# Optimization experiments

Hardware: AMD Instinct MI355X
Metric: run time of the kernel (lower is better)

The kernel has to match this reference:

```python
import jax, jax.numpy as jnp
import numpy as np

N = 50000      # nodes
E = 600000     # edges
F_IN = 128
F_OUT = 128
R = 4          # num_relations
BN_EPS = 1e-5  # PyTorch BatchNorm1d default


def setup_inputs() -> dict:
    key = jax.random.key(0)
    ks = jax.random.split(key, 8)
    s = 1.0 / np.sqrt(F_IN)
    return {
        "x": jax.random.normal(ks[0], (N, F_IN), jnp.float32),
        "edge_index": jax.random.randint(ks[1], (2, E), 0, N),
        "edge_type": jax.random.randint(ks[2], (E,), 0, R),
        "W_self": jax.random.uniform(ks[3], (F_IN, F_OUT), jnp.float32, -s, s),
        "b_self": jnp.zeros((F_OUT,), jnp.float32),
        "W1": jax.random.uniform(ks[4], (R, F_IN, F_OUT), jnp.float32, -s, s),
        "b1": jnp.zeros((R, F_OUT), jnp.float32),
        "gamma": jnp.ones((R, F_OUT), jnp.float32),
        "beta": jnp.zeros((R, F_OUT), jnp.float32),
        "W2": jax.random.uniform(ks[5], (R, F_OUT, F_OUT), jnp.float32, -s, s),
        "b2": jnp.zeros((R, F_OUT), jnp.float32),
    }


def reference(x, edge_index, edge_type, W_self, b_self, W1, b1, gamma, beta, W2, b2):
    row, col = edge_index[0], edge_index[1]
    # Per-relation scatter-add aggregation in one segment_sum pass:
    # segment id = relation * N + destination row.
    seg = edge_type * N + row
    agg = jax.ops.segment_sum(x[col], seg, num_segments=R * N)
    agg = agg.reshape(R, N, F_IN)
    # GIN update with eps=0: h_r = x + agg_r
    h = x[None, :, :] + agg                              # (R, N, F_IN)
    # Per-relation MLP: Linear -> BatchNorm(train stats) -> ReLU -> Linear
    h = jnp.einsum('rnf,rfo->rno', h, W1) + b1[:, None, :]
    mean = jnp.mean(h, axis=1, keepdims=True)
    var = jnp.var(h, axis=1, keepdims=True)              # biased, as in BN
    h = (h - mean) * jax.lax.rsqrt(var + BN_EPS)
    h = h * gamma[:, None, :] + beta[:, None, :]
    h = jax.nn.relu(h)
    h = jnp.einsum('rno,rop->rnp', h, W2) + b2[:, None, :]
    # Self-loop linear plus sum over relations
    return x @ W_self + b_self + jnp.sum(h, axis=0)
```

## Files before the change

kernel.cpp:

```cpp
#include <hip/hip_runtime.h>

#define Nn 50000
#define Ee 600000
#define Rr 4
#define NSEG (Rr * Nn)
#define NBIN 200704
#define BN_EPS 1e-5f
#define ECAP 2048

typedef __bf16 bfrag  __attribute__((ext_vector_type(8)));
typedef float  f32x4  __attribute__((ext_vector_type(4)));

__device__ __forceinline__ unsigned short f2b(float f) {
    union { float f; unsigned int u; } v; v.f = f;
    return (unsigned short)((v.u + 0x7FFFu + ((v.u >> 16) & 1u)) >> 16);
}
__device__ __forceinline__ float b2f(unsigned short u) {
    union { unsigned int u; float f; } v; v.u = ((unsigned int)u) << 16; return v.f;
}

__global__ __launch_bounds__(256) void prep_k(
    const float* __restrict__ x, const float* __restrict__ W1,
    const float* __restrict__ W2, const float* __restrict__ Wself,
    const int* __restrict__ ei, const int* __restrict__ et,
    unsigned int* __restrict__ xb, unsigned short* __restrict__ WT,
    int* __restrict__ hist)
{
    int b = blockIdx.x;
    if (b < 12500) {
        int i = b * 256 + threadIdx.x;
        float2 v = ((const float2*)x)[i];
        xb[i] = ((unsigned int)f2b(v.y) << 16) | f2b(v.x);
    } else if (b < 13076) {
        int idx = (b - 12500) * 256 + threadIdx.x;
        int mat = idx >> 14, rem = idx & 16383;
        int n = rem >> 7, k = rem & 127;
        const float* src = (mat < 4) ? (W1 + mat * 16384)
                         : (mat < 8) ? (W2 + (mat - 4) * 16384) : Wself;
        WT[idx] = f2b(src[k * 128 + n]);
    } else {
        int e = (b - 13076) * 256 + threadIdx.x;
        if (e < Ee) atomicAdd(&hist[et[e] * Nn + ei[e]], 1);
    }
}

__global__ __launch_bounds__(256) void scan1_k(
    const int* __restrict__ hist, int* __restrict__ offs, int* __restrict__ bsum)
{
    int t = threadIdx.x, b = blockIdx.x;
    int base = b * 1024 + t * 4;
    int4 c = *(const int4*)(hist + base);
    int s = c.x + c.y + c.z + c.w;
    __shared__ int tmp[256];
    tmp[t] = s; __syncthreads();
    for (int off = 1; off < 256; off <<= 1) {
        int v = (t >= off) ? tmp[t - off] : 0;
        __syncthreads(); tmp[t] += v; __syncthreads();
    }
    int excl = tmp[t] - s;
    int4 o; o.x = excl; o.y = excl + c.x; o.z = o.y + c.y; o.w = o.z + c.z;
    *(int4*)(offs + base) = o;
    if (t == 255) bsum[b] = tmp[255];
}
__global__ void scan2_k(const int* __restrict__ bsum, int* __restrict__ bscan)
{
    int t = threadIdx.x;
    int s = (t < 196) ? bsum[t] : 0;
    __shared__ int tmp[256];
    tmp[t] = s; __syncthreads();
    for (int off = 1; off < 256; off <<= 1) {
        int v = (t >= off) ? tmp[t - off] : 0;
        __syncthreads(); tmp[t] += v; __syncthreads();
    }
    bscan[t] = tmp[t] - s;
}
__global__ __launch_bounds__(256) void scan3_k(
    int* __restrict__ offs, int* __restrict__ cur, const int* __restrict__ bscan)
{
    int t = threadIdx.x, b = blockIdx.x;
    int add = bscan[b];
    int base = b * 1024 + t * 4;
    int4 o = *(int4*)(offs + base);
    o.x += add; o.y += add; o.z += add; o.w += add;
    *(int4*)(offs + base) = o;
    *(int4*)(cur + base) = o;
}

__global__ __launch_bounds__(256) void fill_k(
    const int* __restrict__ ei, const int* __restrict__ et,
    int* __restrict__ cur, int* __restrict__ ssrc)
{
    int e = blockIdx.x * 256 + threadIdx.x;
    if (e >= Ee) return;
    int bin = et[e] * Nn + ei[e];
    int pos = atomicAdd(&cur[bin], 1);
    ssrc[pos] = ei[Ee + e];
}

__global__ __launch_bounds__(512) void gemm1f_k(
    const unsigned int* __restrict__ xb, const int* __restrict__ offs,
    const int* __restrict__ ssrc, const unsigned short* __restrict__ WT,
    const float* __restrict__ b1, unsigned short* __restrict__ h,
    float* __restrict__ gsum, float* __restrict__ gsq)
{
    const int r  = blockIdx.y;
    const int n0 = blockIdx.x * 128;
    const int t  = threadIdx.x;

    __shared__ __attribute__((aligned(16))) __bf16 As[128][136];
    __shared__ __attribute__((aligned(16))) __bf16 Ws[128][136];
    __shared__ float s_sum[128], s_sq[128];
    __shared__ int s_off[129];
    __shared__ int s_edge[ECAP];

    if (t < 128) { s_sum[t] = 0.f; s_sq[t] = 0.f; }
    const int rows = (Nn - n0 < 128) ? (Nn - n0) : 128;
    if (t <= rows) s_off[t] = offs[r * Nn + n0 + t];
    __syncthreads();

    const int ebeg = s_off[0];
    const int ecnt = s_off[rows] - ebeg;
    const bool inl = (ecnt <= ECAP);
    if (inl) for (int i = t; i < ecnt; i += 512) s_edge[i] = ssrc[ebeg + i];
    {
        const unsigned short* Wr = WT + r * 16384;
        for (int i = t; i < 2048; i += 512) {
            int n = i >> 4, kc = (i & 15) << 3;
            *(uint4*)&Ws[n][kc] = *(const uint4*)(Wr + n * 128 + kc);
        }
    }
    __syncthreads();

    {
        const int row = t >> 2, q = t & 3, gm = n0 + row;
        float acc[32];
        if (gm < Nn) {
            const uint4* xr = (const uint4*)(xb + (size_t)gm * 64 + q * 16);
            uint4 u0 = xr[0], u1 = xr[1], u2 = xr[2], u3 = xr[3];
            unsigned int us[16] = {u0.x,u0.y,u0.z,u0.w, u1.x,u1.y,u1.z,u1.w,
                                   u2.x,u2.y,u2.z,u2.w, u3.x,u3.y,u3.z,u3.w};
#pragma unroll
            for (int j = 0; j < 16; ++j) {
                acc[2*j]   = b2f((unsigned short)(us[j] & 0xFFFF));
                acc[2*j+1] = b2f((unsigned short)(us[j] >> 16));
            }
            int jb = s_off[row] - ebeg, je = s_off[row + 1] - ebeg;
            for (int j = jb; j < je; ++j) {
                int src = inl ? s_edge[j] : ssrc[ebeg + j];
                const uint4* sr = (const uint4*)(xb + (size_t)src * 64 + q * 16);
                uint4 v0 = sr[0], v1 = sr[1], v2 = sr[2], v3 = sr[3];
                unsigned int vs[16] = {v0.x,v0.y,v0.z,v0.w, v1.x,v1.y,v1.z,v1.w,
                                       v2.x,v2.y,v2.z,v2.w, v3.x,v3.y,v3.z,v3.w};
#pragma unroll
                for (int jj = 0; jj < 16; ++jj) {
                    acc[2*jj]   += b2f((unsigned short)(vs[jj] & 0xFFFF));
                    acc[2*jj+1] += b2f((unsigned short)(vs[jj] >> 16));
                }
            }
        } else {
#pragma unroll
            for (int j = 0; j < 32; ++j) acc[j] = 0.f;
        }
        unsigned int pk[16];
#pragma unroll
        for (int j = 0; j < 16; ++j)
            pk[j] = ((unsigned int)f2b(acc[2*j+1]) << 16) | f2b(acc[2*j]);
        uint4* dst = (uint4*)&As[row][q * 32];
        dst[0] = make_uint4(pk[0],  pk[1],  pk[2],  pk[3]);
        dst[1] = make_uint4(pk[4],  pk[5],  pk[6],  pk[7]);
        dst[2] = make_uint4(pk[8],  pk[9],  pk[10], pk[11]);
        dst[3] = make_uint4(pk[12], pk[13], pk[14], pk[15]);
    }
    __syncthreads();

    const int w = t >> 6, l = t & 63, ln = l & 15, quad = l >> 4;
    f32x4 acc2[8];
#pragma unroll
    for (int c = 0; c < 8; ++c) acc2[c] = (f32x4){0.f,0.f,0.f,0.f};
#pragma unroll
    for (int kk = 0; kk < 4; ++kk) {
        int ks = kk * 32 + quad * 8;
        bfrag a = *(const bfrag*)&As[w * 16 + ln][ks];
#pragma unroll
        for (int c = 0; c < 8; ++c) {
            bfrag b = *(const bfrag*)&Ws[c * 16 + ln][ks];
            acc2[c] = __builtin_amdgcn_mfma_f32_16x16x32_bf16(a, b, acc2[c], 0, 0, 0);
        }
    }
    __syncthreads();

#pragma unroll
    for (int c = 0; c < 8; ++c) {
        int col = c * 16 + ln;
        float bias = b1[r * 128 + col];
        float ps = 0.f, pq = 0.f;
#pragma unroll
        for (int reg = 0; reg < 4; ++reg) {
            int lrow = w * 16 + quad * 4 + reg;
            float v = acc2[c][reg] + bias;
            As[lrow][col] = (__bf16)v;
            if (n0 + lrow < Nn) { ps += v; pq += v * v; }
        }
        ps += __shfl_xor(ps, 16); pq += __shfl_xor(pq, 16);
        ps += __shfl_xor(ps, 32); pq += __shfl_xor(pq, 32);
        if (quad == 0) { atomicAdd(&s_sum[col], ps); atomicAdd(&s_sq[col], pq); }
    }
    __syncthreads();

    unsigned short* hr = h + (size_t)r * Nn * 128;
    for (int i = t; i < 2048; i += 512) {
        int m = i >> 4, kc = (i & 15) << 3;
        int gm = n0 + m;
        if (gm < Nn) *(uint4*)(hr + (size_t)gm * 128 + kc) = *(const uint4*)&As[m][kc];
    }
    if (t < 128) {
        atomicAdd(&gsum[r * 128 + t], s_sum[t]);
        atomicAdd(&gsq[r * 128 + t],  s_sq[t]);
    }
}

__global__ void finalize_k(
    const float* __restrict__ gsum, const float* __restrict__ gsq,
    const float* __restrict__ gamma, const float* __restrict__ beta,
    float* __restrict__ coefA, float* __restrict__ coefC)
{
    int i = threadIdx.x;
    float mean = gsum[i] * (1.0f / Nn);
    float var  = gsq[i] * (1.0f / Nn) - mean * mean;
    float a    = gamma[i] * rsqrtf(fmaxf(var, 0.f) + BN_EPS);
    coefA[i] = a;
    coefC[i] = beta[i] - mean * a;
}

__global__ __launch_bounds__(512) void gemm2f_k(
    const unsigned int* __restrict__ xb,
    const unsigned short* __restrict__ h,
    const unsigned short* __restrict__ WT,
    const float* __restrict__ bself, const float* __restrict__ b2,
    const float* __restrict__ coefA, const float* __restrict__ coefC,
    float* __restrict__ out)
{
    const int n0 = blockIdx.x * 128;
    const int t  = threadIdx.x;
    __shared__ __attribute__((aligned(16))) __bf16 As[128][136];
    __shared__ __attribute__((aligned(16))) __bf16 Ws[128][136];

    const int w = t >> 6, l = t & 63, ln = l & 15, quad = l >> 4;
    f32x4 acc2[8];
#pragma unroll
    for (int c = 0; c < 8; ++c) acc2[c] = (f32x4){0.f,0.f,0.f,0.f};

    for (int rr = 0; rr < 5; ++rr) {
        const unsigned short* Wr = WT + (rr < 4 ? (4 + rr) : 8) * 16384;
        for (int i = t; i < 2048; i += 512) {
            int n = i >> 4, kc = (i & 15) << 3;
            *(uint4*)&Ws[n][kc] = *(const uint4*)(Wr + n * 128 + kc);
        }
        if (rr < 4) {
            const unsigned short* hrp = h + (size_t)rr * Nn * 128;
            const float* cA = coefA + rr * 128;
            const float* cC = coefC + rr * 128;
            for (int i = t; i < 2048; i += 512) {
                int m = i >> 4, kc = (i & 15) << 3;
                int gm = n0 + m;
                uint4 hv = make_uint4(0,0,0,0);
                if (gm < Nn) hv = *(const uint4*)(hrp + (size_t)gm * 128 + kc);
                unsigned int hu[4] = {hv.x, hv.y, hv.z, hv.w};
                unsigned int pk[4];
#pragma unroll
                for (int j = 0; j < 4; ++j) {
                    float v0 = fmaxf(cA[kc + 2*j]     * b2f((unsigned short)(hu[j] & 0xFFFF)) + cC[kc + 2*j],     0.f);
                    float v1 = fmaxf(cA[kc + 2*j + 1] * b2f((unsigned short)(hu[j] >> 16))    + cC[kc + 2*j + 1], 0.f);
                    pk[j] = ((unsigned int)f2b(v1) << 16) | f2b(v0);
                }
                *(uint4*)&As[m][kc] = make_uint4(pk[0], pk[1], pk[2], pk[3]);
            }
        } else {
            for (int i = t; i < 2048; i += 512) {
                int m = i >> 4, kc = (i & 15) << 3;
                int gm = n0 + m;
                uint4 v = make_uint4(0, 0, 0, 0);
                if (gm < Nn) v = *(const uint4*)(xb + (size_t)gm * 64 + (kc >> 1));
                *(uint4*)&As[m][kc] = v;
            }
        }
        __syncthreads();
#pragma unroll
        for (int kk = 0; kk < 4; ++kk) {
            int ks = kk * 32 + quad * 8;
            bfrag a = *(const bfrag*)&As[w * 16 + ln][ks];
#pragma unroll
            for (int c = 0; c < 8; ++c) {
                bfrag b = *(const bfrag*)&Ws[c * 16 + ln][ks];
                acc2[c] = __builtin_amdgcn_mfma_f32_16x16x32_bf16(a, b, acc2[c], 0, 0, 0);
            }
        }
        __syncthreads();
    }

    float bias[8];
#pragma unroll
    for (int c = 0; c < 8; ++c) {
        int col = c * 16 + ln;
        bias[c] = bself[col] + b2[col] + b2[128 + col] + b2[256 + col] + b2[384 + col];
    }
    float* fws = (float*)Ws;
    for (int p = 0; p < 2; ++p) {
        if ((w >> 2) == p) {
#pragma unroll
            for (int c = 0; c < 8; ++c) {
                int lrow = (w & 3) * 16 + quad * 4;
                int col  = c * 16 + ln;
#pragma unroll
                for (int reg = 0; reg < 4; ++reg)
                    fws[(lrow + reg) * 132 + col] = acc2[c][reg] + bias[c];
            }
        }
        __syncthreads();
        for (int i = t; i < 2048; i += 512) {
            int m = i >> 5, kc = (i & 31) << 2;
            int gm = n0 + p * 64 + m;
            if (gm < Nn)
                *(float4*)(out + (size_t)gm * 128 + kc) = *(const float4*)&fws[m * 132 + kc];
        }
        __syncthreads();
    }
}

extern "C" void kernel_launch(void* const* d_in, const int* in_sizes, int n_in,
                              void* d_out, int out_size, void* d_ws, size_t ws_size,
                              hipStream_t stream) {
    const float* x     = (const float*)d_in[0];
    const int*   ei    = (const int*)d_in[1];
    const int*   et    = (const int*)d_in[2];
    const float* Wself = (const float*)d_in[3];
    const float* bself = (const float*)d_in[4];
    const float* W1    = (const float*)d_in[5];
    const float* b1    = (const float*)d_in[6];
    const float* gamma = (const float*)d_in[7];
    const float* beta  = (const float*)d_in[8];
    const float* W2    = (const float*)d_in[9];
    const float* b2    = (const float*)d_in[10];
    float* out = (float*)d_out;

    char* ws = (char*)d_ws;
    int*   hist  = (int*)(ws + 0);
    float* gsum  = (float*)(ws + 802816);
    float* gsq   = (float*)(ws + 804864);
    float* coefA = (float*)(ws + 806912);
    float* coefC = (float*)(ws + 808960);
    int*   bsum  = (int*)(ws + 811008);
    int*   bscan = (int*)(ws + 812032);
    int*   offs  = (int*)(ws + 813056);
    int*   cur   = (int*)(ws + 1615872);
    int*   ssrc  = (int*)(ws + 2418688);
    unsigned short* h  = (unsigned short*)(ws + 4818688);
    unsigned int*   xb = (unsigned int*)(ws + 56018688);
    unsigned short* WT = (unsigned short*)(ws + 68818688);

    (void)hipMemsetAsync(ws, 0, 806912, stream);

    const int EB = (Ee + 255) / 256;
    prep_k <<<12500 + 576 + EB, 256, 0, stream>>>(x, W1, W2, Wself, ei, et, xb, WT, hist);
    scan1_k<<<196, 256, 0, stream>>>(hist, offs, bsum);
    scan2_k<<<1, 256, 0, stream>>>(bsum, bscan);
    scan3_k<<<196, 256, 0, stream>>>(offs, cur, bscan);
    fill_k <<<EB, 256, 0, stream>>>(ei, et, cur, ssrc);

    dim3 g1((Nn + 127) / 128, Rr);
    gemm1f_k<<<g1, 512, 0, stream>>>(xb, offs, ssrc, WT, b1, h, gsum, gsq);
    finalize_k<<<1, 512, 0, stream>>>(gsum, gsq, gamma, beta, coefA, coefC);
    gemm2f_k<<<(Nn + 127) / 128, 512, 0, stream>>>(
        xb, h, WT, bself, b2, coefA, coefC, out);
}
```

Measured before the change: 271.1 us.

## Prefetch next relation tiles into registers in gemm2 and unroll edge gather

In the second GEMM kernel, the weight and activation tiles for the next relation are loaded into registers while the MFMA loop for the current relation runs, then written to shared memory after the barrier. This hides global load latency behind compute. The gather loop in the first GEMM now handles two edges per iteration so more independent loads are in flight. Both changes raise register pressure, which could lower occupancy.

Result: slower. 289.6 us (+6.8%).

```diff
diff --git a/kernel.cpp b/kernel.cpp
--- a/kernel.cpp
+++ b/kernel.cpp
@@ -97,6 +97,17 @@
     ssrc[pos] = ei[Ee + e];
 }
 
+#define ACC_QUAD(u0_, u1_, u2_, u3_)                                      \
+    do {                                                                  \
+        unsigned int uu[16] = {u0_.x,u0_.y,u0_.z,u0_.w, u1_.x,u1_.y,u1_.z,u1_.w, \
+                               u2_.x,u2_.y,u2_.z,u2_.w, u3_.x,u3_.y,u3_.z,u3_.w}; \
+        _Pragma("unroll")                                                 \
+        for (int jj = 0; jj < 16; ++jj) {                                 \
+            acc[2*jj]   += b2f((unsigned short)(uu[jj] & 0xFFFF));        \
+            acc[2*jj+1] += b2f((unsigned short)(uu[jj] >> 16));           \
+        }                                                                 \
+    } while (0)
+
 __global__ __launch_bounds__(512) void gemm1f_k(
     const unsigned int* __restrict__ xb, const int* __restrict__ offs,
     const int* __restrict__ ssrc, const unsigned short* __restrict__ WT,
@@ -137,25 +148,26 @@
         if (gm < Nn) {
             const uint4* xr = (const uint4*)(xb + (size_t)gm * 64 + q * 16);
             uint4 u0 = xr[0], u1 = xr[1], u2 = xr[2], u3 = xr[3];
-            unsigned int us[16] = {u0.x,u0.y,u0.z,u0.w, u1.x,u1.y,u1.z,u1.w,
-                                   u2.x,u2.y,u2.z,u2.w, u3.x,u3.y,u3.z,u3.w};
-#pragma unroll
-            for (int j = 0; j < 16; ++j) {
-                acc[2*j]   = b2f((unsigned short)(us[j] & 0xFFFF));
-                acc[2*j+1] = b2f((unsigned short)(us[j] >> 16));
-            }
+#pragma unroll
+            for (int j = 0; j < 32; ++j) acc[j] = 0.f;
+            ACC_QUAD(u0, u1, u2, u3);
             int jb = s_off[row] - ebeg, je = s_off[row + 1] - ebeg;
-            for (int j = jb; j < je; ++j) {
-                int src = inl ? s_edge[j] : ssrc[ebeg + j];
-                const uint4* sr = (const uint4*)(xb + (size_t)src * 64 + q * 16);
-                uint4 v0 = sr[0], v1 = sr[1], v2 = sr[2], v3 = sr[3];
-                unsigned int vs[16] = {v0.x,v0.y,v0.z,v0.w, v1.x,v1.y,v1.z,v1.w,
-                                       v2.x,v2.y,v2.z,v2.w, v3.x,v3.y,v3.z,v3.w};
-#pragma unroll
-                for (int jj = 0; jj < 16; ++jj) {
-                    acc[2*jj]   += b2f((unsigned short)(vs[jj] & 0xFFFF));
-                    acc[2*jj+1] += b2f((unsigned short)(vs[jj] >> 16));
-                }
+            int j = jb;
+            for (; j + 2 <= je; j += 2) {
+                int s0 = inl ? s_edge[j]     : ssrc[ebeg + j];
+                int s1 = inl ? s_edge[j + 1] : ssrc[ebeg + j + 1];
+                const uint4* p0 = (const uint4*)(xb + (size_t)s0 * 64 + q * 16);
+                const uint4* p1 = (const uint4*)(xb + (size_t)s1 * 64 + q * 16);
+                uint4 a0 = p0[0], a1 = p0[1], a2 = p0[2], a3 = p0[3];
+                uint4 b0 = p1[0], b1v = p1[1], b2v = p1[2], b3 = p1[3];
+                ACC_QUAD(a0, a1, a2, a3);
+                ACC_QUAD(b0, b1v, b2v, b3);
+            }
+            if (j < je) {
+                int s0 = inl ? s_edge[j] : ssrc[ebeg + j];
+                const uint4* p0 = (const uint4*)(xb + (size_t)s0 * 64 + q * 16);
+                uint4 a0 = p0[0], a1 = p0[1], a2 = p0[2], a3 = p0[3];
+                ACC_QUAD(a0, a1, a2, a3);
             }
         } else {
 #pragma unroll
@@ -250,41 +262,72 @@
 #pragma unroll
     for (int c = 0; c < 8; ++c) acc2[c] = (f32x4){0.f,0.f,0.f,0.f};
 
+    int cn[4], ck[4], cm[4], cgm[4];
+#pragma unroll
+    for (int k = 0; k < 4; ++k) {
+        int i = t + 512 * k;
+        cn[k] = i >> 4; ck[k] = (i & 15) << 3;
+        cm[k] = cn[k];  cgm[k] = n0 + cm[k];
+    }
+
+    uint4 wreg[4], areg[4];
+    {
+        const unsigned short* Wr = WT + 4 * 16384;
+        const unsigned short* hrp = h;
+#pragma unroll
+        for (int k = 0; k < 4; ++k) {
+            wreg[k] = *(const uint4*)(Wr + cn[k] * 128 + ck[k]);
+            areg[k] = (cgm[k] < Nn) ? *(const uint4*)(hrp + (size_t)cgm[k] * 128 + ck[k])
+                                    : make_uint4(0,0,0,0);
+        }
+    }
+
     for (int rr = 0; rr < 5; ++rr) {
-        const unsigned short* Wr = WT + (rr < 4 ? (4 + rr) : 8) * 16384;
-        for (int i = t; i < 2048; i += 512) {
-            int n = i >> 4, kc = (i & 15) << 3;
-            *(uint4*)&Ws[n][kc] = *(const uint4*)(Wr + n * 128 + kc);
-        }
         if (rr < 4) {
-            const unsigned short* hrp = h + (size_t)rr * Nn * 128;
             const float* cA = coefA + rr * 128;
             const float* cC = coefC + rr * 128;
-            for (int i = t; i < 2048; i += 512) {
-                int m = i >> 4, kc = (i & 15) << 3;
-                int gm = n0 + m;
-                uint4 hv = make_uint4(0,0,0,0);
-                if (gm < Nn) hv = *(const uint4*)(hrp + (size_t)gm * 128 + kc);
-                unsigned int hu[4] = {hv.x, hv.y, hv.z, hv.w};
+#pragma unroll
+            for (int k = 0; k < 4; ++k) {
+                unsigned int hu[4] = {areg[k].x, areg[k].y, areg[k].z, areg[k].w};
                 unsigned int pk[4];
 #pragma unroll
                 for (int j = 0; j < 4; ++j) {
-                    float v0 = fmaxf(cA[kc + 2*j]     * b2f((unsigned short)(hu[j] & 0xFFFF)) + cC[kc + 2*j],     0.f);
-                    float v1 = fmaxf(cA[kc + 2*j + 1] * b2f((unsigned short)(hu[j] >> 16))    + cC[kc + 2*j + 1], 0.f);
+                    int kc = ck[k] + 2 * j;
+                    float v0 = fmaxf(cA[kc]     * b2f((unsigned short)(hu[j] & 0xFFFF)) + cC[kc],     0.f);
+                    float v1 = fmaxf(cA[kc + 1] * b2f((unsigned short)(hu[j] >> 16))    + cC[kc + 1], 0.f);
                     pk[j] = ((unsigned int)f2b(v1) << 16) | f2b(v0);
                 }
-                *(uint4*)&As[m][kc] = make_uint4(pk[0], pk[1], pk[2], pk[3]);
+                *(uint4*)&As[cm[k]][ck[k]] = make_uint4(pk[0], pk[1], pk[2], pk[3]);
+                *(uint4*)&Ws[cn[k]][ck[k]] = wreg[k];
             }
         } else {
-            for (int i = t; i < 2048; i += 512) {
-                int m = i >> 4, kc = (i & 15) << 3;
-                int gm = n0 + m;
-                uint4 v = make_uint4(0, 0, 0, 0);
-                if (gm < Nn) v = *(const uint4*)(xb + (size_t)gm * 64 + (kc >> 1));
-                *(uint4*)&As[m][kc] = v;
+#pragma unroll
+            for (int k = 0; k < 4; ++k) {
+                *(uint4*)&As[cm[k]][ck[k]] = areg[k];
+                *(uint4*)&Ws[cn[k]][ck[k]] = wreg[k];
             }
         }
         __syncthreads();
+
+        if (rr < 4) {
+            const unsigned short* Wr = (rr < 3) ? (WT + (5 + rr) * 16384) : (WT + 8 * 16384);
+#pragma unroll
+            for (int k = 0; k < 4; ++k)
+                wreg[k] = *(const uint4*)(Wr + cn[k] * 128 + ck[k]);
+            if (rr < 3) {
+                const unsigned short* hrp = h + (size_t)(rr + 1) * Nn * 128;
+#pragma unroll
+                for (int k = 0; k < 4; ++k)
+                    areg[k] = (cgm[k] < Nn) ? *(const uint4*)(hrp + (size_t)cgm[k] * 128 + ck[k])
+                                            : make_uint4(0,0,0,0);
+            } else {
+#pragma unroll
+                for (int k = 0; k < 4; ++k)
+                    areg[k] = (cgm[k] < Nn) ? *(const uint4*)(xb + (size_t)cgm[k] * 64 + (ck[k] >> 1))
+                                            : make_uint4(0,0,0,0);
+            }
+        }
+
 #pragma unroll
         for (int kk = 0; kk < 4; ++kk) {
             int ks = kk * 32 + quad * 8;
```

## Parallelize edge gather over edges with LDS float atomics, halve row tile

Applied to the files above, without the earlier changes.

The per-node gather, where each thread looped over one node's edges, becomes an edge-parallel loop. Each thread takes half an edge's feature row and accumulates it into an fp32 shared-memory tile with atomicAdd. The sorted edge list now stores (src,dst) pairs so each edge knows its destination row, and the row tile shrinks from 128 to 64 with 8 waves splitting the output columns. This is meant to fix load imbalance from uneven node degrees and raise gather parallelism, at the cost of many LDS atomics, doubled edge-list traffic, bf16 conversion at MFMA operand load, and more blocks that each reload W. Summation order now varies between runs.

Measured after the change: 662.7 us. 144% more time.

```diff
diff --git a/kernel.cpp b/kernel.cpp
--- a/kernel.cpp
+++ b/kernel.cpp
@@ -3,10 +3,8 @@
 #define Nn 50000
 #define Ee 600000
 #define Rr 4
-#define NSEG (Rr * Nn)
 #define NBIN 200704
 #define BN_EPS 1e-5f
-#define ECAP 2048
 
 typedef __bf16 bfrag  __attribute__((ext_vector_type(8)));
 typedef float  f32x4  __attribute__((ext_vector_type(4)));
@@ -88,40 +86,35 @@
 
 __global__ __launch_bounds__(256) void fill_k(
     const int* __restrict__ ei, const int* __restrict__ et,
-    int* __restrict__ cur, int* __restrict__ ssrc)
+    int* __restrict__ cur, int2* __restrict__ spair)
 {
     int e = blockIdx.x * 256 + threadIdx.x;
     if (e >= Ee) return;
-    int bin = et[e] * Nn + ei[e];
+    int dst = ei[e];
+    int bin = et[e] * Nn + dst;
     int pos = atomicAdd(&cur[bin], 1);
-    ssrc[pos] = ei[Ee + e];
+    spair[pos] = make_int2(ei[Ee + e], dst);
 }
 
 __global__ __launch_bounds__(512) void gemm1f_k(
     const unsigned int* __restrict__ xb, const int* __restrict__ offs,
-    const int* __restrict__ ssrc, const unsigned short* __restrict__ WT,
+    const int2* __restrict__ spair, const unsigned short* __restrict__ WT,
     const float* __restrict__ b1, unsigned short* __restrict__ h,
     float* __restrict__ gsum, float* __restrict__ gsq)
 {
     const int r  = blockIdx.y;
-    const int n0 = blockIdx.x * 128;
+    const int n0 = blockIdx.x * 64;
     const int t  = threadIdx.x;
 
-    __shared__ __attribute__((aligned(16))) __bf16 As[128][136];
+    __shared__ __attribute__((aligned(16))) float  Asf[64][130];
     __shared__ __attribute__((aligned(16))) __bf16 Ws[128][136];
     __shared__ float s_sum[128], s_sq[128];
-    __shared__ int s_off[129];
-    __shared__ int s_edge[ECAP];
 
     if (t < 128) { s_sum[t] = 0.f; s_sq[t] = 0.f; }
-    const int rows = (Nn - n0 < 128) ? (Nn - n0) : 128;
-    if (t <= rows) s_off[t] = offs[r * Nn + n0 + t];
-    __syncthreads();
-
-    const int ebeg = s_off[0];
-    const int ecnt = s_off[rows] - ebeg;
-    const bool inl = (ecnt <= ECAP);
-    if (inl) for (int i = t; i < ecnt; i += 512) s_edge[i] = ssrc[ebeg + i];
+    const int rows = (Nn - n0 < 64) ? (Nn - n0) : 64;
+    const int ebeg = offs[r * Nn + n0];
+    const int eend = offs[r * Nn + n0 + rows];
+
     {
         const unsigned short* Wr = WT + r * 16384;
         for (int i = t; i < 2048; i += 512) {
@@ -129,76 +122,85 @@
             *(uint4*)&Ws[n][kc] = *(const uint4*)(Wr + n * 128 + kc);
         }
     }
+    {
+        int row = t >> 3, q = t & 7;
+        int gm = n0 + row;
+        uint4 a = make_uint4(0,0,0,0), b = make_uint4(0,0,0,0);
+        if (gm < Nn) {
+            const uint4* xr = (const uint4*)(xb + (size_t)gm * 64 + q * 8);
+            a = xr[0]; b = xr[1];
+        }
+        unsigned int uu[8] = {a.x,a.y,a.z,a.w, b.x,b.y,b.z,b.w};
+        float* bas = &Asf[row][q * 16];
+#pragma unroll
+        for (int j = 0; j < 8; ++j) {
+            bas[2*j]   = b2f((unsigned short)(uu[j] & 0xFFFF));
+            bas[2*j+1] = b2f((unsigned short)(uu[j] >> 16));
+        }
+    }
     __syncthreads();
 
     {
-        const int row = t >> 2, q = t & 3, gm = n0 + row;
-        float acc[32];
-        if (gm < Nn) {
-            const uint4* xr = (const uint4*)(xb + (size_t)gm * 64 + q * 16);
-            uint4 u0 = xr[0], u1 = xr[1], u2 = xr[2], u3 = xr[3];
-            unsigned int us[16] = {u0.x,u0.y,u0.z,u0.w, u1.x,u1.y,u1.z,u1.w,
-                                   u2.x,u2.y,u2.z,u2.w, u3.x,u3.y,u3.z,u3.w};
-#pragma unroll
-            for (int j = 0; j < 16; ++j) {
-                acc[2*j]   = b2f((unsigned short)(us[j] & 0xFFFF));
-                acc[2*j+1] = b2f((unsigned short)(us[j] >> 16));
-            }
-            int jb = s_off[row] - ebeg, je = s_off[row + 1] - ebeg;
-            for (int j = jb; j < je; ++j) {
-                int src = inl ? s_edge[j] : ssrc[ebeg + j];
-                const uint4* sr = (const uint4*)(xb + (size_t)src * 64 + q * 16);
-                uint4 v0 = sr[0], v1 = sr[1], v2 = sr[2], v3 = sr[3];
-                unsigned int vs[16] = {v0.x,v0.y,v0.z,v0.w, v1.x,v1.y,v1.z,v1.w,
-                                       v2.x,v2.y,v2.z,v2.w, v3.x,v3.y,v3.z,v3.w};
-#pragma unroll
-                for (int jj = 0; jj < 16; ++jj) {
-                    acc[2*jj]   += b2f((unsigned short)(vs[jj] & 0xFFFF));
-                    acc[2*jj+1] += b2f((unsigned short)(vs[jj] >> 16));
-                }
-            }
-        } else {
-#pragma unroll
-            for (int j = 0; j < 32; ++j) acc[j] = 0.f;
-        }
-        unsigned int pk[16];
-#pragma unroll
-        for (int j = 0; j < 16; ++j)
-            pk[j] = ((unsigned int)f2b(acc[2*j+1]) << 16) | f2b(acc[2*j]);
-        uint4* dst = (uint4*)&As[row][q * 32];
-        dst[0] = make_uint4(pk[0],  pk[1],  pk[2],  pk[3]);
-        dst[1] = make_uint4(pk[4],  pk[5],  pk[6],  pk[7]);
-        dst[2] = make_uint4(pk[8],  pk[9],  pk[10], pk[11]);
-        dst[3] = make_uint4(pk[12], pk[13], pk[14], pk[15]);
+        const int units = 2 * (eend - ebeg);
+        for (int u = t; u < units; u += 512) {
+            int e  = ebeg + (u >> 1);
+            int hf = u & 1;
+            int2 sd = spair[e];
+            const uint4* p = (const uint4*)(xb + (size_t)sd.x * 64 + hf * 32);
+            uint4 q0 = p[0], q1 = p[1], q2 = p[2], q3 = p[3];
+            uint4 q4 = p[4], q5 = p[5], q6 = p[6], q7 = p[7];
+            float* bas = &Asf[sd.y - n0][hf << 6];
+            unsigned int qq[32] = {q0.x,q0.y,q0.z,q0.w, q1.x,q1.y,q1.z,q1.w,
+                                   q2.x,q2.y,q2.z,q2.w, q3.x,q3.y,q3.z,q3.w,
+                                   q4.x,q4.y,q4.z,q4.w, q5.x,q5.y,q5.z,q5.w,
+                                   q6.x,q6.y,q6.z,q6.w, q7.x,q7.y,q7.z,q7.w};
+#pragma unroll
+            for (int j = 0; j < 32; ++j) {
+                atomicAdd(&bas[2*j],   b2f((unsigned short)(qq[j] & 0xFFFF)));
+                atomicAdd(&bas[2*j+1], b2f((unsigned short)(qq[j] >> 16)));
+            }
+        }
     }
     __syncthreads();
 
     const int w = t >> 6, l = t & 63, ln = l & 15, quad = l >> 4;
-    f32x4 acc2[8];
-#pragma unroll
-    for (int c = 0; c < 8; ++c) acc2[c] = (f32x4){0.f,0.f,0.f,0.f};
+    const int rg = w & 3, ch = w >> 2;
+    f32x4 acc2[4];
+#pragma unroll
+    for (int c = 0; c < 4; ++c) acc2[c] = (f32x4){0.f,0.f,0.f,0.f};
 #pragma unroll
     for (int kk = 0; kk < 4; ++kk) {
         int ks = kk * 32 + quad * 8;
-        bfrag a = *(const bfrag*)&As[w * 16 + ln][ks];
-#pragma unroll
-        for (int c = 0; c < 8; ++c) {
-            bfrag b = *(const bfrag*)&Ws[c * 16 + ln][ks];
+        int arow = rg * 16 + ln;
+        float2 f0 = *(const float2*)&Asf[arow][ks];
+        float2 f1 = *(const float2*)&Asf[arow][ks + 2];
+        float2 f2 = *(const float2*)&Asf[arow][ks + 4];
+        float2 f3 = *(const float2*)&Asf[arow][ks + 6];
+        bfrag a;
+        a[0] = (__bf16)f0.x; a[1] = (__bf16)f0.y;
+        a[2] = (__bf16)f1.x; a[3] = (__bf16)f1.y;
+        a[4] = (__bf16)f2.x; a[5] = (__bf16)f2.y;
+        a[6] = (__bf16)f3.x; a[7] = (__bf16)f3.y;
+#pragma unroll
+        for (int c = 0; c < 4; ++c) {
+            int col = ch * 64 + c * 16 + ln;
+            bfrag b = *(const bfrag*)&Ws[col][ks];
             acc2[c] = __builtin_amdgcn_mfma_f32_16x16x32_bf16(a, b, acc2[c], 0, 0, 0);
         }
     }
     __syncthreads();
 
-#pragma unroll
-    for (int c = 0; c < 8; ++c) {
-        int col = c * 16 + ln;
+    __bf16 (*Hs)[136] = (__bf16(*)[136])Ws;
+#pragma unroll
+    for (int c = 0; c < 4; ++c) {
+        int col = ch * 64 + c * 16 + ln;
         float bias = b1[r * 128 + col];
         float ps = 0.f, pq = 0.f;
 #pragma unroll
         for (int reg = 0; reg < 4; ++reg) {
-            int lrow = w * 16 + quad * 4 + reg;
+            int lrow = rg * 16 + quad * 4 + reg;
             float v = acc2[c][reg] + bias;
-            As[lrow][col] = (__bf16)v;
+            Hs[lrow][col] = (__bf16)v;
             if (n0 + lrow < Nn) { ps += v; pq += v * v; }
         }
         ps += __shfl_xor(ps, 16); pq += __shfl_xor(pq, 16);
@@ -208,10 +210,10 @@
     __syncthreads();
 
     unsigned short* hr = h + (size_t)r * Nn * 128;
-    for (int i = t; i < 2048; i += 512) {
+    for (int i = t; i < 1024; i += 512) {
         int m = i >> 4, kc = (i & 15) << 3;
         int gm = n0 + m;
-        if (gm < Nn) *(uint4*)(hr + (size_t)gm * 128 + kc) = *(const uint4*)&As[m][kc];
+        if (gm < Nn) *(uint4*)(hr + (size_t)gm * 128 + kc) = *(const uint4*)&Hs[m][kc];
     }
     if (t < 128) {
         atomicAdd(&gsum[r * 128 + t], s_sum[t]);
@@ -353,10 +355,10 @@
     int*   bscan = (int*)(ws + 812032);
     int*   offs  = (int*)(ws + 813056);
     int*   cur   = (int*)(ws + 1615872);
-    int*   ssrc  = (int*)(ws + 2418688);
-    unsigned short* h  = (unsigned short*)(ws + 4818688);
-    unsigned int*   xb = (unsigned int*)(ws + 56018688);
-    unsigned short* WT = (unsigned short*)(ws + 68818688);
+    int2*  spair = (int2*)(ws + 2418688);
+    unsigned short* h  = (unsigned short*)(ws + 7218688);
+    unsigned int*   xb = (unsigned int*)(ws + 58418688);
+    unsigned short* WT = (unsigned short*)(ws + 71218688);
 
     (void)hipMemsetAsync(ws, 0, 806912, stream);
 
@@ -365,10 +367,10 @@
     scan1_k<<<196, 256, 0, stream>>>(hist, offs, bsum);
     scan2_k<<<1, 256, 0, stream>>>(bsum, bscan);
     scan3_k<<<196, 256, 0, stream>>>(offs, cur, bscan);
-    fill_k <<<EB, 256, 0, stream>>>(ei, et, cur, ssrc);
-
-    dim3 g1((Nn + 127) / 128, Rr);
-    gemm1f_k<<<g1, 512, 0, stream>>>(xb, offs, ssrc, WT, b1, h, gsum, gsq);
+    fill_k <<<EB, 256, 0, stream>>>(ei, et, cur, spair);
+
+    dim3 g1((Nn + 63) / 64, Rr);
+    gemm1f_k<<<g1, 512, 0, stream>>>(xb, offs, spair, WT, b1, h, gsum, gsq);
     finalize_k<<<1, 512, 0, stream>>>(gsum, gsq, gamma, beta, coefA, coefC);
     gemm2f_k<<<(Nn + 127) / 128, 512, 0, stream>>>(
         xb, h, WT, bself, b2, coefA, coefC, out);
```
